# Kernel tuning notes

Measured on AMD Instinct MI355X. Metric: run time of the kernel, lower is better.

## Reference

```python
import jax, jax.numpy as jnp
import numpy as np
from jax import lax

B, H, W, C, K, R, CB = 2, 128, 128, 256, 64, 8, 256


def _conv(x, w, b=None, pad=1, lhs_dil=None, groups=1):
    out = lax.conv_general_dilated(x, w, (1, 1), [(pad, pad), (pad, pad)],
                                   lhs_dilation=lhs_dil, feature_group_count=groups,
                                   dimension_numbers=('NCHW', 'OIHW', 'NCHW'))
    return out if b is None else out + b[None, :, None, None]


def _silu(x):
    return x * jax.nn.sigmoid(x)


def _fuse(l0, l1, l2, p1w, p1b, p2w, p3w):
    # proj1: Conv(k=3)+SiLU (BN folded); proj2/proj3: grouped ConvTranspose2d as lhs-dilated grouped convs
    a = _silu(_conv(l0, p1w, p1b))
    b2 = _conv(l1, p2w, pad=2, lhs_dil=(2, 2), groups=CB)  # ConvT(2CB->CB, k4, s2, p1, g=CB)
    b3 = _conv(l2, p3w, pad=5, lhs_dil=(4, 4), groups=CB)  # ConvT(4CB->CB, k8, s4, p2, g=CB)
    return a + b2 + b3


def _corr_map(emb, trk):
    # emb: [H,W,C], trk: [K,C]; cosine-similarity correlation with local argmax radius masking
    e = emb / jnp.maximum(jnp.linalg.norm(emb, axis=-1, keepdims=True), 1e-12)
    t = trk / jnp.maximum(jnp.linalg.norm(trk, axis=-1, keepdims=True), 1e-12)
    y = jnp.maximum(jnp.einsum('hwc,kc->khw', e, t), 0.0)  # torch.where(y>0, y, 0)
    idx = jnp.argmax(y.reshape(K, -1), axis=1)             # first max, like torch.nonzero(...)[0]
    ai, aj = idx // W, idx % W
    rows = jnp.arange(H)[None, :, None]
    cols = jnp.arange(W)[None, None, :]
    m = ((rows >= (ai[:, None, None] - R)) & (rows < (ai[:, None, None] + R)) &
         (cols >= (aj[:, None, None] - R)) & (cols < (aj[:, None, None] + R)))
    s = jnp.sum(y * m, axis=0)
    return s / jnp.max(s)


def setup_inputs():
    key = jax.random.key(0)
    ks = jax.random.split(key, 32)
    r = lambda i, shp, s=0.02: jax.random.normal(ks[i], shp, jnp.float32) * s
    z = lambda n: jnp.zeros((n,), jnp.float32)
    return dict(
        id_embeding=jax.random.normal(ks[0], (B, H, W, C), jnp.float32),
        tracklets=jax.random.normal(ks[1], (B, K, C), jnp.float32),
        l0=jax.random.normal(ks[2], (B, CB, H, W), jnp.float32),
        l1=jax.random.normal(ks[3], (B, 2 * CB, H // 2, W // 2), jnp.float32),
        l2=jax.random.normal(ks[4], (B, 4 * CB, H // 4, W // 4), jnp.float32),
        b_p1w=r(5, (CB, CB, 3, 3)), b_p1b=z(CB),
        b_p2w=r(6, (CB, 2, 4, 4)), b_p3w=r(7, (CB, 4, 8, 8)),
        b_c1w=r(8, (CB, CB, 3, 3)), b_c1b=z(CB),
        b_c2w=r(9, (4, CB, 3, 3)), b_c2b=z(4),
        h_p1w=r(10, (CB, CB, 3, 3)), h_p1b=z(CB),
        h_p2w=r(11, (CB, 2, 4, 4)), h_p3w=r(12, (CB, 4, 8, 8)),
        h_c1aw=r(13, (CB, 1, 3, 3), 0.1), h_c1ab=z(CB),
        h_c1bw=r(14, (1, CB, 3, 3)), h_c1bb=z(1),
        h_c2aw=r(15, (CB, CB, 3, 3)), h_c2ab=z(CB),
        h_c2bw=r(16, (CB, CB, 3, 3)), h_c2bb=z(CB),
        h_c2cw=r(17, (1, CB, 3, 3)), h_c2cb=z(1),
    )


def reference(id_embeding, tracklets, l0, l1, l2,
              b_p1w, b_p1b, b_p2w, b_p3w, b_c1w, b_c1b, b_c2w, b_c2b,
              h_p1w, h_p1b, h_p2w, h_p3w,
              h_c1aw, h_c1ab, h_c1bw, h_c1bb,
              h_c2aw, h_c2ab, h_c2bw, h_c2bb, h_c2cw, h_c2cb):
    # correlation map per batch -> x_F [B,1,H,W]
    x_F = jax.vmap(_corr_map)(id_embeding, tracklets)[:, None]
    # recheck_Box head
    xd_box = _fuse(l0, l1, l2, b_p1w, b_p1b, b_p2w, b_p3w)
    xb = _silu(_conv(xd_box, b_c1w, b_c1b))
    siambox = jnp.transpose(_conv(xb, b_c2w, b_c2b), (0, 2, 3, 1))  # [B,H,W,4]
    # recheck_heatmap head
    xd_hm = _fuse(l0, l1, l2, h_p1w, h_p1b, h_p2w, h_p3w)
    xf = _conv(_silu(_conv(x_F, h_c1aw, h_c1ab)), h_c1bw, h_c1bb)   # [B,1,H,W]
    t = xf * xd_hm                                                  # broadcast over CB channels
    t = _silu(_conv(t, h_c2aw, h_c2ab))
    t = _silu(_conv(t, h_c2bw, h_c2bb))
    hmmap = jax.nn.sigmoid(_conv(t, h_c2cw, h_c2cb))                # [B,1,H,W]
    return (hmmap, siambox)
```

## Files before the change

kernel.cpp:

```cpp
#include <hip/hip_runtime.h>
#include <math.h>

#define HH 128
#define WW 128
#define HWSZ 16384
#define CC 256
#define KK 64
#define BB 2

typedef __bf16 bf16x8_t __attribute__((ext_vector_type(8)));
typedef float  f32x4_t  __attribute__((ext_vector_type(4)));

__device__ __forceinline__ float silu_f(float v) { return v / (1.f + expf(-v)); }
__device__ __forceinline__ float sigm_f(float v) { return 1.f / (1.f + expf(-v)); }

__device__ __forceinline__ float b2f(unsigned short u) {
    union { unsigned int i; float f; } x; x.i = ((unsigned int)u) << 16; return x.f;
}
__device__ __forceinline__ unsigned short f2b(float f) {
    union { float f; unsigned int i; } x; x.f = f;
    unsigned int r = x.i + 0x7FFFu + ((x.i >> 16) & 1u);
    return (unsigned short)(r >> 16);
}
__device__ __forceinline__ float u2f(unsigned int u) {
    union { unsigned int i; float f; } x; x.i = u; return x.f;
}

__global__ __launch_bounds__(256) void cvt_nhwc_kernel(const float* __restrict__ in,
                                                       unsigned short* __restrict__ out) {
    __shared__ float T[32][128];
    const int tid = threadIdx.x;
    const int y = blockIdx.x & 127;
    const int b = blockIdx.x >> 7;
    const float* inb = in + (size_t)b * CC * HWSZ + y * 128;
    unsigned short* outb = out + ((size_t)b * HWSZ + (size_t)y * 128) * CC;

    for (int c0 = 0; c0 < CC; c0 += 32) {
        __syncthreads();
        {
            int cl = tid >> 3;
            int xq = tid & 7;
            const float4* src = (const float4*)(inb + (size_t)(c0 + cl) * HWSZ);
            float4* dst = (float4*)&T[cl][0];
            #pragma unroll
            for (int j = 0; j < 4; j++) dst[xq * 4 + j] = src[xq * 4 + j];
        }
        __syncthreads();
        {
            int x = tid & 127, ch = tid >> 7;
            union { unsigned short u[16]; uint4 v[2]; } pk;
            #pragma unroll
            for (int j = 0; j < 16; j++) pk.u[j] = f2b(T[ch * 16 + j][x]);
            uint4* dst = (uint4*)&outb[(size_t)x * CC + c0 + ch * 16];
            dst[0] = pk.v[0];
            dst[1] = pk.v[1];
        }
    }
}

#define WTSZ (9 * 8 * 256 * 32)
__global__ __launch_bounds__(256) void wprep5_kernel(const float* __restrict__ w0,
                                                     const float* __restrict__ w1,
                                                     const float* __restrict__ w2,
                                                     const float* __restrict__ w3,
                                                     const float* __restrict__ w4,
                                                     unsigned short* __restrict__ wtbase) {
    const float* ws[5] = {w0, w1, w2, w3, w4};
    int set = blockIdx.y;
    const float* w = ws[set];
    int idx = blockIdx.x * 256 + threadIdx.x;
    int e   = idx & 7;
    int co  = (idx >> 3) & 255;
    int g   = (idx >> 11) & 3;
    int v   = idx >> 13;
    int cb  = v / 9;
    int t   = v - cb * 9;
    wtbase[(size_t)set * WTSZ + idx] = f2b(w[((size_t)co * 256 + cb * 32 + g * 8 + e) * 9 + t]);
}

#define EPAD 260
__global__ __launch_bounds__(256) void ycorr_kernel(const float* __restrict__ emb,
                                                    const float* __restrict__ trk,
                                                    float* __restrict__ y) {
    __shared__ __align__(16) float E[64 * EPAD];
    __shared__ __align__(16) float T[64 * EPAD];
    __shared__ float SE[64];
    __shared__ float ST[64];

    const int tid = threadIdx.x;
    const int b   = blockIdx.y;
    const int hw0 = blockIdx.x * 64;

    const float4* esrc = (const float4*)(emb + ((size_t)b * HWSZ + hw0) * CC);
    #pragma unroll
    for (int i = 0; i < 16; i++) {
        int q  = tid + i * 256;
        int px = q >> 6, c4 = q & 63;
        *(float4*)&E[px * EPAD + c4 * 4] = esrc[(size_t)px * 64 + c4];
    }
    const float4* tsrc = (const float4*)(trk + (size_t)b * KK * CC);
    #pragma unroll
    for (int i = 0; i < 16; i++) {
        int q = tid + i * 256;
        int k = q >> 6, c4 = q & 63;
        *(float4*)&T[k * EPAD + c4 * 4] = tsrc[(size_t)k * 64 + c4];
    }
    __syncthreads();

    if (tid < 64) {
        float ss = 0.f;
        const float4* ep = (const float4*)&E[tid * EPAD];
        #pragma unroll 8
        for (int c4 = 0; c4 < 64; c4++) {
            float4 v = ep[c4];
            ss += v.x * v.x + v.y * v.y + v.z * v.z + v.w * v.w;
        }
        SE[tid] = 1.f / fmaxf(sqrtf(ss), 1e-12f);
    } else if (tid < 128) {
        float ss = 0.f;
        const float4* tp = (const float4*)&T[(tid - 64) * EPAD];
        #pragma unroll 8
        for (int c4 = 0; c4 < 64; c4++) {
            float4 v = tp[c4];
            ss += v.x * v.x + v.y * v.y + v.z * v.z + v.w * v.w;
        }
        ST[tid - 64] = 1.f / fmaxf(sqrtf(ss), 1e-12f);
    }
    __syncthreads();

    const int pg = tid & 15;
    const int kg = tid >> 4;

    float acc[4][4];
    #pragma unroll
    for (int jp = 0; jp < 4; jp++)
        #pragma unroll
        for (int jk = 0; jk < 4; jk++) acc[jp][jk] = 0.f;

    const float* Ep[4];
    const float* Tp[4];
    #pragma unroll
    for (int jp = 0; jp < 4; jp++) Ep[jp] = &E[(jp * 16 + pg) * EPAD];
    #pragma unroll
    for (int jk = 0; jk < 4; jk++) Tp[jk] = &T[(jk * 16 + kg) * EPAD];

    #pragma unroll 2
    for (int c4 = 0; c4 < 64; ++c4) {
        float4 e[4], t[4];
        #pragma unroll
        for (int jp = 0; jp < 4; jp++) e[jp] = *(const float4*)(Ep[jp] + c4 * 4);
        #pragma unroll
        for (int jk = 0; jk < 4; jk++) t[jk] = *(const float4*)(Tp[jk] + c4 * 4);
        #define DOT4(a, t) (fmaf(a.w, t.w, fmaf(a.z, t.z, fmaf(a.y, t.y, a.x * t.x))))
        #pragma unroll
        for (int jp = 0; jp < 4; jp++)
            #pragma unroll
            for (int jk = 0; jk < 4; jk++)
                acc[jp][jk] += DOT4(e[jp], t[jk]);
        #undef DOT4
    }

    #pragma unroll
    for (int jp = 0; jp < 4; jp++) {
        int px = jp * 16 + pg;
        float se = SE[px];
        #pragma unroll
        for (int jk = 0; jk < 4; jk++) {
            int k = jk * 16 + kg;
            y[((size_t)b * KK + k) * HWSZ + hw0 + px] = fmaxf(acc[jp][jk], 0.f) * se * ST[k];
        }
    }
}

__global__ __launch_bounds__(256) void argmax_kernel(const float* __restrict__ y,
                                                     int* __restrict__ idxout,
                                                     unsigned int* __restrict__ umax) {
    int bk = blockIdx.x;
    int t = threadIdx.x;
    if (bk == 0 && t < BB) umax[t] = 0u;
    const float* p = y + (size_t)bk * HWSZ;
    float best = -1.f; int bi = 1 << 30;
    for (int i = t; i < HWSZ; i += 256) {
        float v = p[i];
        if (v > best) { best = v; bi = i; }
    }
    __shared__ float sv[256];
    __shared__ int   si[256];
    sv[t] = best; si[t] = bi;
    __syncthreads();
    for (int s = 128; s > 0; s >>= 1) {
        if (t < s) {
            float v2 = sv[t + s]; int i2 = si[t + s];
            if (v2 > sv[t] || (v2 == sv[t] && i2 < si[t])) { sv[t] = v2; si[t] = i2; }
        }
        __syncthreads();
    }
    if (t == 0) idxout[bk] = si[0];
}

__global__ __launch_bounds__(256) void smap_kernel(const float* __restrict__ y,
                                                   const int* __restrict__ idx,
                                                   float* __restrict__ s,
                                                   unsigned int* __restrict__ umax) {
    int b  = blockIdx.y;
    int hw = blockIdx.x * 256 + threadIdx.x;
    int h  = hw >> 7, w = hw & 127;
    __shared__ int ai[KK], aj[KK];
    if (threadIdx.x < KK) {
        int v = idx[b * KK + threadIdx.x];
        ai[threadIdx.x] = v >> 7;
        aj[threadIdx.x] = v & 127;
    }
    __syncthreads();
    const float* yb = y + (size_t)b * KK * HWSZ;
    float acc = 0.f;
    #pragma unroll 8
    for (int k = 0; k < KK; k++) {
        float v = yb[(size_t)k * HWSZ + hw];
        bool in = (h >= ai[k] - 8) && (h < ai[k] + 8) && (w >= aj[k] - 8) && (w < aj[k] + 8);
        acc += in ? v : 0.f;
    }
    s[(size_t)b * HWSZ + hw] = acc;

    __shared__ float sm[256];
    sm[threadIdx.x] = acc;
    __syncthreads();
    for (int st = 128; st > 0; st >>= 1) {
        if (threadIdx.x < st) sm[threadIdx.x] = fmaxf(sm[threadIdx.x], sm[threadIdx.x + st]);
        __syncthreads();
    }
    if (threadIdx.x == 0) {
        union { float f; unsigned int i; } x; x.f = sm[0];
        atomicMax(&umax[b], x.i);
    }
}

template <int HEADS>
__global__ __launch_bounds__(256) void deconv_kernel(const float* __restrict__ l1,
                                                     const float* __restrict__ l2,
                                                     const float* __restrict__ w2a,
                                                     const float* __restrict__ w3a,
                                                     const float* __restrict__ w2b,
                                                     const float* __restrict__ w3b,
                                                     unsigned short* __restrict__ outA,
                                                     unsigned short* __restrict__ outB) {
    __shared__ float L1[2][64][64];
    __shared__ float L2[4][32][32];

    const int tid = threadIdx.x;
    const int g   = blockIdx.x & 255;
    const int b   = blockIdx.x >> 8;

    const float4* l1b = (const float4*)(l1 + ((size_t)b * 2 * CC + 2 * g) * 4096);
    float4* L1p = (float4*)&L1[0][0][0];
    #pragma unroll
    for (int i = 0; i < 8; i++) L1p[tid + i * 256] = l1b[tid + i * 256];
    const float4* l2b = (const float4*)(l2 + ((size_t)b * 4 * CC + 4 * g) * 1024);
    float4* L2p = (float4*)&L2[0][0][0];
    #pragma unroll
    for (int i = 0; i < 4; i++) L2p[tid + i * 256] = l2b[tid + i * 256];

    const int x    = tid & 127;
    const int ytop = tid >> 7;

    const int pxo = x & 1, pyo = ytop & 1;
    const int mx0 = (x + pxo - 2) >> 1;
    const int dy2 = (ytop + pyo - 2) >> 1;
    const bool nok0 = (unsigned)mx0 < 64u;
    const bool nok1 = (unsigned)(mx0 + 1) < 64u;
    const int nc0 = mx0 & 63, nc1 = (mx0 + 1) & 63;

    const int px3 = (5 - (x & 3)) & 3;
    const int n30 = (x + px3 - 5) >> 2;
    const bool n3ok0 = (unsigned)n30 < 32u;
    const bool n3ok1 = (unsigned)(n30 + 1) < 32u;
    const int n3c0 = n30 & 31, n3c1 = (n30 + 1) & 31;
    int dy3[2], py3v[2];
    #pragma unroll
    for (int ph = 0; ph < 2; ph++) {
        int py3 = (5 - ((ytop + 2 * ph) & 3)) & 3;
        py3v[ph] = py3;
        dy3[ph] = (2 * ph + ytop + py3 - 5) >> 2;
    }

    __syncthreads();

    const float* w2s[2] = {w2a, w2b};
    const float* w3s[2] = {w3a, w3b};
    unsigned short* outs[2] = {outA, outB};

    #pragma unroll 1
    for (int hd = 0; hd < HEADS; ++hd) {
        const float* w2g = w2s[hd] + (size_t)g * 32;
        const float* w3g = w3s[hd] + (size_t)g * 256;

        float W2[2][2][2];
        #pragma unroll
        for (int ci = 0; ci < 2; ci++)
            #pragma unroll
            for (int a = 0; a < 2; a++)
                #pragma unroll
                for (int c = 0; c < 2; c++)
                    W2[ci][a][c] = w2g[ci * 16 + (pyo + 2 * a) * 4 + (pxo + 2 * c)];
        float W3[2][4][2][2];
        #pragma unroll
        for (int ph = 0; ph < 2; ph++)
            #pragma unroll
            for (int ci = 0; ci < 4; ci++)
                #pragma unroll
                for (int a = 0; a < 2; a++)
                    #pragma unroll
                    for (int c = 0; c < 2; c++)
                        W3[ph][ci][a][c] = w3g[ci * 64 + (py3v[ph] + 4 * a) * 8 + (px3 + 4 * c)];

        unsigned short* outb = outs[hd] + ((size_t)b * CC + g) * HWSZ;

        #pragma unroll 2
        for (int ii = 0; ii < 32; ++ii) {
            #pragma unroll
            for (int ph = 0; ph < 2; ph++) {
                const int i = 2 * ii + ph;
                float acc = 0.f;
                {
                    const int m0 = i + dy2;
                    #pragma unroll
                    for (int a = 0; a < 2; a++) {
                        int m = m0 + a;
                        bool mok = (unsigned)m < 64u;
                        int mc = m & 63;
                        #pragma unroll
                        for (int ci = 0; ci < 2; ci++) {
                            float v0 = (mok && nok0) ? L1[ci][mc][nc0] : 0.f;
                            float v1 = (mok && nok1) ? L1[ci][mc][nc1] : 0.f;
                            acc = fmaf(W2[ci][a][0], v0, acc);
                            acc = fmaf(W2[ci][a][1], v1, acc);
                        }
                    }
                }
                {
                    const int m0 = ii + dy3[ph];
                    #pragma unroll
                    for (int a = 0; a < 2; a++) {
                        int m = m0 + a;
                        bool mok = (unsigned)m < 32u;
                        int mc = m & 31;
                        #pragma unroll
                        for (int ci = 0; ci < 4; ci++) {
                            float v0 = (mok && n3ok0) ? L2[ci][mc][n3c0] : 0.f;
                            float v1 = (mok && n3ok1) ? L2[ci][mc][n3c1] : 0.f;
                            acc = fmaf(W3[ph][ci][a][0], v0, acc);
                            acc = fmaf(W3[ph][ci][a][1], v1, acc);
                        }
                    }
                }
                outb[(size_t)i * 256 + tid] = f2b(acc);
            }
        }
    }
}

template <int ADDB, int MULF>
__device__ __forceinline__ void conv_mfma_body(
    int y0, int co0, int b,
    const unsigned short* __restrict__ in,
    const unsigned short* __restrict__ wt,
    const float* __restrict__ bias,
    const unsigned short* __restrict__ addb,
    const float* __restrict__ xf,
    unsigned short* __restrict__ out,
    unsigned short (*Alds)[3 * 130 * 32])
{
    const int tid  = threadIdx.x;
    const int lane = tid & 63;
    const int wv   = tid >> 6;
    const int wco  = wv >> 1;
    const int wpx  = wv & 1;
    const int l15  = lane & 15;
    const int kg   = lane >> 4;

    const unsigned short* inb = in + (size_t)b * HWSZ * CC;
    const float* xfb = MULF ? (xf + (size_t)b * HWSZ) : nullptr;
    const unsigned short* wp = wt + (size_t)kg * 2048 + (size_t)(co0 + wco * 64 + l15) * 8;

    int ach[3][4];
    #pragma unroll
    for (int tl = 0; tl < 3; tl++)
        #pragma unroll
        for (int f = 0; f < 4; f++) {
            int px = wpx * 64 + f * 16 + l15 + tl;
            ach[tl][f] = (px * 4 + (kg ^ ((px >> 1) & 3))) * 8;
        }

    f32x4_t acc[4][4];
    #pragma unroll
    for (int i = 0; i < 4; i++)
        #pragma unroll
        for (int j = 0; j < 4; j++)
            acc[i][j] = (f32x4_t){0.f, 0.f, 0.f, 0.f};

    if (tid < 48) {
        int q4 = tid & 3;
        int hp = (tid >> 2) & 1;
        int r  = (tid >> 3) % 3;
        int bi = tid / 24;
        int px = hp ? 129 : 0;
        int chunk = (r * 130 + px) * 4 + (q4 ^ ((px >> 1) & 3));
        *reinterpret_cast<uint4*>(&Alds[bi][chunk * 8]) = make_uint4(0u, 0u, 0u, 0u);
    }

    uint4 streg[6];
    float sxf[6];

    auto load_A = [&](int cb) {
        #pragma unroll
        for (int i = 0; i < 6; i++) {
            int q   = tid + i * 256;
            int q4  = q & 3;
            int pxi = (q >> 2) & 127;
            int r   = q >> 9;
            int gy  = y0 - 1 + r;
            uint4 v = make_uint4(0u, 0u, 0u, 0u);
            float fxv = 0.f;
            if ((unsigned)gy < 128u) {
                v = *reinterpret_cast<const uint4*>(
                        inb + ((size_t)(gy * 128 + pxi)) * CC + cb * 32 + q4 * 8);
                if (MULF) fxv = xfb[gy * 128 + pxi];
            }
            streg[i] = v;
            if (MULF) sxf[i] = fxv;
        }
    };
    auto write_A = [&](int bufi) {
        #pragma unroll
        for (int i = 0; i < 6; i++) {
            int q   = tid + i * 256;
            int q4  = q & 3;
            int pxi = (q >> 2) & 127;
            int r   = q >> 9;
            int px  = pxi + 1;
            int chunk = (r * 130 + px) * 4 + (q4 ^ ((px >> 1) & 3));
            uint4 v = streg[i];
            if (MULF) {
                union { unsigned short u[8]; uint4 w; } pk;
                pk.w = v;
                float fm = sxf[i];
                #pragma unroll
                for (int e = 0; e < 8; e++) pk.u[e] = f2b(b2f(pk.u[e]) * fm);
                v = pk.w;
            }
            *reinterpret_cast<uint4*>(&Alds[bufi][chunk * 8]) = v;
        }
    };

    load_A(0);
    write_A(0);

    bf16x8_t W[3][4], P[2][4];
    #pragma unroll
    for (int f = 0; f < 4; f++) W[0][f] = *reinterpret_cast<const bf16x8_t*>(wp + f * 128);
    #pragma unroll
    for (int f = 0; f < 4; f++) W[1][f] = *reinterpret_cast<const bf16x8_t*>(wp + 8192 + f * 128);

    __syncthreads();
    #pragma unroll
    for (int f = 0; f < 4; f++)
        P[0][f] = *reinterpret_cast<const bf16x8_t*>(&Alds[0][ach[0][f]]);

    for (int cb = 0; cb < 8; ++cb) {
        const int bufi = cb & 1;
        if (cb + 1 < 8) load_A(cb + 1);
        const unsigned short* wcb = wp + (size_t)cb * 73728;
        #pragma unroll
        for (int t = 0; t < 9; ++t) {
            if (cb < 7 || t < 7) {
                #pragma unroll
                for (int f = 0; f < 4; f++)
                    W[(t + 2) % 3][f] = *reinterpret_cast<const bf16x8_t*>(
                        wcb + (t + 2) * 8192 + f * 128);
            }
            if (t < 8) {
                const int aoff = ((t + 1) / 3) * 4160;
                #pragma unroll
                for (int f = 0; f < 4; f++)
                    P[(t + 1) & 1][f] = *reinterpret_cast<const bf16x8_t*>(
                        &Alds[bufi][aoff + ach[(t + 1) % 3][f]]);
            }
            __builtin_amdgcn_sched_barrier(0);
            #pragma unroll
            for (int cf = 0; cf < 4; cf++)
                #pragma unroll
                for (int pf = 0; pf < 4; pf++)
                    acc[cf][pf] = __builtin_amdgcn_mfma_f32_16x16x32_bf16(
                        W[t % 3][cf], P[t & 1][pf], acc[cf][pf], 0, 0, 0);
        }
        if (cb + 1 < 8) write_A(bufi ^ 1);
        __syncthreads();
        if (cb + 1 < 8) {
            #pragma unroll
            for (int f = 0; f < 4; f++)
                P[0][f] = *reinterpret_cast<const bf16x8_t*>(&Alds[(cb + 1) & 1][ach[0][f]]);
        }
    }

    size_t outB = ((size_t)b * HWSZ + (size_t)y0 * 128) * CC;
    #pragma unroll
    for (int cf = 0; cf < 4; cf++) {
        int co = co0 + wco * 64 + cf * 16 + kg * 4;
        float bs0 = bias[co], bs1 = bias[co + 1], bs2 = bias[co + 2], bs3 = bias[co + 3];
        #pragma unroll
        for (int pf = 0; pf < 4; pf++) {
            int x = wpx * 64 + pf * 16 + l15;
            float v0 = silu_f(acc[cf][pf][0] + bs0);
            float v1 = silu_f(acc[cf][pf][1] + bs1);
            float v2 = silu_f(acc[cf][pf][2] + bs2);
            float v3 = silu_f(acc[cf][pf][3] + bs3);
            if (ADDB) {
                size_t ab = ((size_t)b * CC + co) * HWSZ + (size_t)y0 * 128 + x;
                v0 += b2f(addb[ab]);
                v1 += b2f(addb[ab + HWSZ]);
                v2 += b2f(addb[ab + 2 * HWSZ]);
                v3 += b2f(addb[ab + 3 * HWSZ]);
            }
            union { unsigned short u[4]; uint2 v; } pk;
            pk.u[0] = f2b(v0); pk.u[1] = f2b(v1); pk.u[2] = f2b(v2); pk.u[3] = f2b(v3);
            *reinterpret_cast<uint2*>(&out[outB + (size_t)x * CC + co]) = pk.v;
        }
    }
}

template <int ADDB, int MULF>
__global__ __launch_bounds__(256, 2) void conv_mfma_kernel(
    const unsigned short* __restrict__ in,
    const unsigned short* __restrict__ wt,
    const float* __restrict__ bias,
    const unsigned short* __restrict__ addb,
    const float* __restrict__ xf,
    unsigned short* __restrict__ out)
{
    __shared__ __align__(16) unsigned short Alds[2][3 * 130 * 32];
    const int l   = (blockIdx.x & 7) * 64 + (blockIdx.x >> 3);
    const int y0  = l >> 2;
    const int co0 = ((l >> 1) & 1) * 128;
    const int b   = l & 1;
    conv_mfma_body<ADDB, MULF>(y0, co0, b, in, wt, bias, addb, xf, out, Alds);
}

__global__ __launch_bounds__(256, 2) void conv_mfma_dual_kernel(
    const unsigned short* __restrict__ in,
    const unsigned short* __restrict__ wt2set,
    const float* __restrict__ biasB,
    const float* __restrict__ biasH,
    const unsigned short* __restrict__ addbB,
    const unsigned short* __restrict__ addbH,
    unsigned short* __restrict__ outB,
    unsigned short* __restrict__ outH)
{
    __shared__ __align__(16) unsigned short Alds[2][3 * 130 * 32];
    const int l    = (blockIdx.x & 7) * 128 + (blockIdx.x >> 3);
    const int y0   = l >> 3;
    const int c3   = l & 7;
    const int head = c3 >> 2;
    const int co0  = ((c3 >> 1) & 1) * 128;
    const int b    = c3 & 1;
    conv_mfma_body<1, 0>(y0, co0, b,
                         in,
                         wt2set + (size_t)head * WTSZ,
                         head ? biasH : biasB,
                         head ? addbH : addbB,
                         nullptr,
                         head ? outH : outB,
                         Alds);
}

__global__ __launch_bounds__(256) void conv_c1a_kernel(const float* __restrict__ s,
                                                       const unsigned int* __restrict__ umax,
                                                       const float* __restrict__ w,
                                                       const float* __restrict__ bias,
                                                       unsigned short* __restrict__ out) {
    __shared__ float W[2304];
    __shared__ float S[3][34];

    const int tid = threadIdx.x;
    const int idx = blockIdx.x;
    const int b   = idx >> 9;
    const int seg = idx & 511;
    const int y   = seg >> 2;
    const int x0  = (seg & 3) * 32;

    for (int i = tid; i < 2304; i += 256) W[i] = w[i];
    if (tid < 102) {
        int r = tid / 34, xx = tid - r * 34;
        int gy = y - 1 + r, gx = x0 - 1 + xx;
        S[r][xx] = ((unsigned)gy < 128u && (unsigned)gx < 128u)
                       ? s[(size_t)b * HWSZ + gy * 128 + gx] : 0.f;
    }
    __syncthreads();

    const float im = 1.f / u2f(umax[b]);
    const int cog = tid >> 5;
    const int px  = tid & 31;

    float sv[9];
    #pragma unroll
    for (int r = 0; r < 3; r++)
        #pragma unroll
        for (int d = 0; d < 3; d++)
            sv[r * 3 + d] = S[r][px + d];

    unsigned short* op =
        &out[((size_t)b * HWSZ + (size_t)y * 128 + x0 + px) * CC + cog * 32];
    #pragma unroll
    for (int q = 0; q < 4; q++) {
        union { unsigned short u[8]; uint4 v; } pk;
        #pragma unroll
        for (int j = 0; j < 8; j++) {
            int co = cog * 32 + q * 8 + j;
            float a = 0.f;
            #pragma unroll
            for (int t = 0; t < 9; t++) a = fmaf(W[co * 9 + t], sv[t], a);
            pk.u[j] = f2b(silu_f(a * im + bias[co]));
        }
        *reinterpret_cast<uint4*>(op + q * 8) = pk.v;
    }
}

template <int COUT, int MODE>
__global__ __launch_bounds__(256) void small_conv_kernel(
    const unsigned short* __restrict__ in,
    const float* __restrict__ w,
    const float* __restrict__ bias,
    float* __restrict__ out)
{
    __shared__ float WL[COUT * 9 * 32 * 12];

    const int tid = threadIdx.x;
    for (int i = tid; i < COUT * 2304; i += 256) {
        int e = i & 7;
        int g = (i >> 3) & 31;
        int rest = i >> 8;
        int t = rest % 9;
        int co = rest / 9;
        WL[((co * 9 + t) * 32 + g) * 12 + e] = w[((size_t)co * 256 + g * 8 + e) * 9 + t];
    }
    __syncthreads();

    const int lane = tid & 63;
    const int wv   = tid >> 6;
    const int c32  = lane & 31;
    const int ps   = lane >> 5;
    const int grp  = blockIdx.x * 4 + wv;
    const int base = grp * 4;
    const int b    = base >> 14;
    const int pix  = base & (HWSZ - 1);
    const int y    = pix >> 7;
    const int x0   = pix & 127;
    const int p0x  = x0 + 2 * ps;

    const unsigned short* inb = in + (size_t)b * HWSZ * CC;

    uint4 d[3][4];
    #pragma unroll
    for (int r = 0; r < 3; r++) {
        int gy = y - 1 + r;
        #pragma unroll
        for (int cx = 0; cx < 4; cx++) {
            int gx = p0x - 1 + cx;
            uint4 v = make_uint4(0u, 0u, 0u, 0u);
            if ((unsigned)gy < 128u && (unsigned)gx < 128u)
                v = *reinterpret_cast<const uint4*>(
                        inb + ((size_t)(gy * 128 + gx)) * CC + c32 * 8);
            d[r][cx] = v;
        }
    }

    float acc[2][COUT];
    #pragma unroll
    for (int p = 0; p < 2; p++)
        #pragma unroll
        for (int c = 0; c < COUT; c++) acc[p][c] = 0.f;

    #pragma unroll
    for (int r = 0; r < 3; r++) {
        float f[4][8];
        #pragma unroll
        for (int cx = 0; cx < 4; cx++) {
            union { unsigned short u[8]; uint4 v; } pk;
            pk.v = d[r][cx];
            #pragma unroll
            for (int e = 0; e < 8; e++) f[cx][e] = b2f(pk.u[e]);
        }
        #pragma unroll
        for (int dx = 0; dx < 3; dx++) {
            #pragma unroll
            for (int co = 0; co < COUT; co++) {
                int bse = ((co * 9 + r * 3 + dx) * 32 + c32) * 12;
                float4 wa = *(const float4*)&WL[bse];
                float4 wb = *(const float4*)&WL[bse + 4];
                #pragma unroll
                for (int p = 0; p < 2; p++) {
                    const float* ff = f[dx + p];
                    float a = acc[p][co];
                    a = fmaf(ff[0], wa.x, a); a = fmaf(ff[1], wa.y, a);
                    a = fmaf(ff[2], wa.z, a); a = fmaf(ff[3], wa.w, a);
                    a = fmaf(ff[4], wb.x, a); a = fmaf(ff[5], wb.y, a);
                    a = fmaf(ff[6], wb.z, a); a = fmaf(ff[7], wb.w, a);
                    acc[p][co] = a;
                }
            }
        }
    }

    #pragma unroll
    for (int m = 1; m <= 16; m <<= 1)
        #pragma unroll
        for (int p = 0; p < 2; p++)
            #pragma unroll
            for (int co = 0; co < COUT; co++)
                acc[p][co] += __shfl_xor(acc[p][co], m);

    if (c32 == 0) {
        #pragma unroll
        for (int p = 0; p < 2; p++) {
            size_t pixidx = (size_t)base + 2 * ps + p;
            if (MODE == 0) {
                ((float4*)out)[pixidx] = make_float4(
                    acc[p][0] + bias[0],
                    acc[p][COUT > 1 ? 1 : 0] + bias[COUT > 1 ? 1 : 0],
                    acc[p][COUT > 2 ? 2 : 0] + bias[COUT > 2 ? 2 : 0],
                    acc[p][COUT > 3 ? 3 : 0] + bias[COUT > 3 ? 3 : 0]);
            } else if (MODE == 1) {
                out[pixidx] = acc[p][0] + bias[0];
            } else {
                out[pixidx] = sigm_f(acc[p][0] + bias[0]);
            }
        }
    }
}

extern "C" void kernel_launch(void* const* d_in, const int* in_sizes, int n_in,
                              void* d_out, int out_size, void* d_ws, size_t ws_size,
                              hipStream_t stream) {
    const float* emb    = (const float*)d_in[0];
    const float* trk    = (const float*)d_in[1];
    const float* l0     = (const float*)d_in[2];
    const float* l1     = (const float*)d_in[3];
    const float* l2     = (const float*)d_in[4];
    const float* b_p1w  = (const float*)d_in[5];
    const float* b_p1b  = (const float*)d_in[6];
    const float* b_p2w  = (const float*)d_in[7];
    const float* b_p3w  = (const float*)d_in[8];
    const float* b_c1w  = (const float*)d_in[9];
    const float* b_c1b  = (const float*)d_in[10];
    const float* b_c2w  = (const float*)d_in[11];
    const float* b_c2b  = (const float*)d_in[12];
    const float* h_p1w  = (const float*)d_in[13];
    const float* h_p1b  = (const float*)d_in[14];
    const float* h_p2w  = (const float*)d_in[15];
    const float* h_p3w  = (const float*)d_in[16];
    const float* h_c1aw = (const float*)d_in[17];
    const float* h_c1ab = (const float*)d_in[18];
    const float* h_c1bw = (const float*)d_in[19];
    const float* h_c1bb = (const float*)d_in[20];
    const float* h_c2aw = (const float*)d_in[21];
    const float* h_c2ab = (const float*)d_in[22];
    const float* h_c2bw = (const float*)d_in[23];
    const float* h_c2bb = (const float*)d_in[24];
    const float* h_c2cw = (const float*)d_in[25];
    const float* h_c2cb = (const float*)d_in[26];

    float* outp = (float*)d_out;

    const size_t ACT = (size_t)BB * CC * HWSZ;
    const size_t WT  = (size_t)WTSZ;
    const size_t SMALLS = 131400;

    unsigned short* l0nh = (unsigned short*)d_ws;
    unsigned short* wtP  = l0nh + ACT;
    unsigned short* bufA = wtP + 5 * WT;
    unsigned short* bufB = bufA + ACT;
    unsigned short* bufC = bufB + ACT;
    float* sbuf   = (float*)(bufC + ACT);
    float* xfb    = sbuf + (size_t)BB * HWSZ;
    unsigned int* umax = (unsigned int*)(xfb + (size_t)BB * HWSZ);
    int*   idxb   = (int*)(umax + 2);
    unsigned short* bufD = bufC + ACT + SMALLS;
    float* ybuf   = (float*)bufB;

    const size_t NEED = (size_t)(bufD + ACT - l0nh) * sizeof(unsigned short);
    const bool fast = ws_size >= NEED;

    cvt_nhwc_kernel<<<BB * 128, 256, 0, stream>>>(l0, l0nh);
    wprep5_kernel<<<dim3((unsigned)(WT / 256), 5), 256, 0, stream>>>(
        b_p1w, h_p1w, b_c1w, h_c2aw, h_c2bw, wtP);

    ycorr_kernel<<<dim3(256, BB), 256, 0, stream>>>(emb, trk, ybuf);
    argmax_kernel<<<BB * KK, 256, 0, stream>>>(ybuf, idxb, umax);
    smap_kernel<<<dim3(64, BB), 256, 0, stream>>>(ybuf, idxb, sbuf, umax);

    if (fast) {
        deconv_kernel<2><<<BB * CC, 256, 0, stream>>>(l1, l2, b_p2w, b_p3w, h_p2w, h_p3w,
                                                      bufA, bufD);
        conv_mfma_dual_kernel<<<1024, 256, 0, stream>>>(l0nh, wtP, b_p1b, h_p1b,
                                                        bufA, bufD, bufB, bufC);
        conv_mfma_kernel<0, 0><<<512, 256, 0, stream>>>(bufB, wtP + 2 * WT, b_c1b,
                                                        nullptr, nullptr, bufA);
        small_conv_kernel<4, 0><<<2048, 256, 0, stream>>>(bufA, b_c2w, b_c2b,
                                                          outp + BB * HWSZ);
        conv_c1a_kernel<<<1024, 256, 0, stream>>>(sbuf, umax, h_c1aw, h_c1ab, bufB);
        small_conv_kernel<1, 1><<<2048, 256, 0, stream>>>(bufB, h_c1bw, h_c1bb, xfb);
        conv_mfma_kernel<0, 1><<<512, 256, 0, stream>>>(bufC, wtP + 3 * WT, h_c2ab,
                                                        nullptr, xfb, bufA);
        conv_mfma_kernel<0, 0><<<512, 256, 0, stream>>>(bufA, wtP + 4 * WT, h_c2bb,
                                                        nullptr, nullptr, bufB);
        small_conv_kernel<1, 2><<<2048, 256, 0, stream>>>(bufB, h_c2cw, h_c2cb, outp);
    } else {
        deconv_kernel<1><<<BB * CC, 256, 0, stream>>>(l1, l2, b_p2w, b_p3w,
                                                      nullptr, nullptr, bufA, nullptr);
        conv_mfma_kernel<1, 0><<<512, 256, 0, stream>>>(l0nh, wtP, b_p1b, bufA,
                                                        nullptr, bufB);
        conv_mfma_kernel<0, 0><<<512, 256, 0, stream>>>(bufB, wtP + 2 * WT, b_c1b,
                                                        nullptr, nullptr, bufC);
        small_conv_kernel<4, 0><<<2048, 256, 0, stream>>>(bufC, b_c2w, b_c2b,
                                                          outp + BB * HWSZ);
        deconv_kernel<1><<<BB * CC, 256, 0, stream>>>(l1, l2, h_p2w, h_p3w,
                                                      nullptr, nullptr, bufA, nullptr);
        conv_mfma_kernel<1, 0><<<512, 256, 0, stream>>>(l0nh, wtP + 1 * WT, h_p1b, bufA,
                                                        nullptr, bufB);
        conv_c1a_kernel<<<1024, 256, 0, stream>>>(sbuf, umax, h_c1aw, h_c1ab, bufC);
        small_conv_kernel<1, 1><<<2048, 256, 0, stream>>>(bufC, h_c1bw, h_c1bb, xfb);
        conv_mfma_kernel<0, 1><<<512, 256, 0, stream>>>(bufB, wtP + 3 * WT, h_c2ab,
                                                        nullptr, xfb, bufA);
        conv_mfma_kernel<0, 0><<<512, 256, 0, stream>>>(bufA, wtP + 4 * WT, h_c2bb,
                                                        nullptr, nullptr, bufC);
        small_conv_kernel<1, 2><<<2048, 256, 0, stream>>>(bufC, h_c2cw, h_c2cb, outp);
    }
}
```

Before: 400.3 us.

## Merge two independent 3x3 MFMA convs into one launch and single-buffer LDS

Adds a combined kernel that runs the box-head c1 conv and the heatmap-head c2a conv (with the xf multiply) in one 1024-block grid, reordering the launch sequence so the xf producers run first. The A-tile LDS staging buffer drops from double to single buffering, with extra barriers around the write, which halves shared memory per block to raise occupancy. The cost is that global-to-LDS writes no longer overlap MFMA work from the previous channel block, so there are more synchronisation stalls.

```diff
diff --git a/kernel.cpp b/kernel.cpp
--- a/kernel.cpp
+++ b/kernel.cpp
@@ -368,7 +368,7 @@
     const unsigned short* __restrict__ addb,
     const float* __restrict__ xf,
     unsigned short* __restrict__ out,
-    unsigned short (*Alds)[3 * 130 * 32])
+    unsigned short* __restrict__ Alds)
 {
     const int tid  = threadIdx.x;
     const int lane = tid & 63;
@@ -398,14 +398,13 @@
         for (int j = 0; j < 4; j++)
             acc[i][j] = (f32x4_t){0.f, 0.f, 0.f, 0.f};
 
-    if (tid < 48) {
+    if (tid < 24) {
         int q4 = tid & 3;
         int hp = (tid >> 2) & 1;
-        int r  = (tid >> 3) % 3;
-        int bi = tid / 24;
+        int r  = tid >> 3;
         int px = hp ? 129 : 0;
         int chunk = (r * 130 + px) * 4 + (q4 ^ ((px >> 1) & 3));
-        *reinterpret_cast<uint4*>(&Alds[bi][chunk * 8]) = make_uint4(0u, 0u, 0u, 0u);
+        *reinterpret_cast<uint4*>(&Alds[chunk * 8]) = make_uint4(0u, 0u, 0u, 0u);
     }
 
     uint4 streg[6];
@@ -430,7 +429,7 @@
             if (MULF) sxf[i] = fxv;
         }
     };
-    auto write_A = [&](int bufi) {
+    auto write_A = [&]() {
         #pragma unroll
         for (int i = 0; i < 6; i++) {
             int q   = tid + i * 256;
@@ -448,12 +447,12 @@
                 for (int e = 0; e < 8; e++) pk.u[e] = f2b(b2f(pk.u[e]) * fm);
                 v = pk.w;
             }
-            *reinterpret_cast<uint4*>(&Alds[bufi][chunk * 8]) = v;
+            *reinterpret_cast<uint4*>(&Alds[chunk * 8]) = v;
         }
     };
 
     load_A(0);
-    write_A(0);
+    write_A();
 
     bf16x8_t W[3][4], P[2][4];
     #pragma unroll
@@ -464,10 +463,9 @@
     __syncthreads();
     #pragma unroll
     for (int f = 0; f < 4; f++)
-        P[0][f] = *reinterpret_cast<const bf16x8_t*>(&Alds[0][ach[0][f]]);
+        P[0][f] = *reinterpret_cast<const bf16x8_t*>(&Alds[ach[0][f]]);
 
     for (int cb = 0; cb < 8; ++cb) {
-        const int bufi = cb & 1;
         if (cb + 1 < 8) load_A(cb + 1);
         const unsigned short* wcb = wp + (size_t)cb * 73728;
         #pragma unroll
@@ -483,7 +481,7 @@
                 #pragma unroll
                 for (int f = 0; f < 4; f++)
                     P[(t + 1) & 1][f] = *reinterpret_cast<const bf16x8_t*>(
-                        &Alds[bufi][aoff + ach[(t + 1) % 3][f]]);
+                        &Alds[aoff + ach[(t + 1) % 3][f]]);
             }
             __builtin_amdgcn_sched_barrier(0);
             #pragma unroll
@@ -493,12 +491,13 @@
                     acc[cf][pf] = __builtin_amdgcn_mfma_f32_16x16x32_bf16(
                         W[t % 3][cf], P[t & 1][pf], acc[cf][pf], 0, 0, 0);
         }
-        if (cb + 1 < 8) write_A(bufi ^ 1);
-        __syncthreads();
         if (cb + 1 < 8) {
+            __syncthreads();
+            write_A();
+            __syncthreads();
             #pragma unroll
             for (int f = 0; f < 4; f++)
-                P[0][f] = *reinterpret_cast<const bf16x8_t*>(&Alds[(cb + 1) & 1][ach[0][f]]);
+                P[0][f] = *reinterpret_cast<const bf16x8_t*>(&Alds[ach[0][f]]);
         }
     }
 
@@ -537,7 +536,7 @@
     const float* __restrict__ xf,
     unsigned short* __restrict__ out)
 {
-    __shared__ __align__(16) unsigned short Alds[2][3 * 130 * 32];
+    __shared__ __align__(16) unsigned short Alds[3 * 130 * 32];
     const int l   = (blockIdx.x & 7) * 64 + (blockIdx.x >> 3);
     const int y0  = l >> 2;
     const int co0 = ((l >> 1) & 1) * 128;
@@ -555,7 +554,7 @@
     unsigned short* __restrict__ outB,
     unsigned short* __restrict__ outH)
 {
-    __shared__ __align__(16) unsigned short Alds[2][3 * 130 * 32];
+    __shared__ __align__(16) unsigned short Alds[3 * 130 * 32];
     const int l    = (blockIdx.x & 7) * 128 + (blockIdx.x >> 3);
     const int y0   = l >> 3;
     const int c3   = l & 7;
@@ -570,6 +569,30 @@
                          nullptr,
                          head ? outH : outB,
                          Alds);
+}
+
+__global__ __launch_bounds__(256, 2) void conv_mfma_dualmix_kernel(
+    const unsigned short* __restrict__ in0,
+    const unsigned short* __restrict__ in1,
+    const unsigned short* __restrict__ wt0,
+    const unsigned short* __restrict__ wt1,
+    const float* __restrict__ bias0,
+    const float* __restrict__ bias1,
+    const float* __restrict__ xf,
+    unsigned short* __restrict__ out0,
+    unsigned short* __restrict__ out1)
+{
+    __shared__ __align__(16) unsigned short Alds[3 * 130 * 32];
+    const int l    = (blockIdx.x & 7) * 128 + (blockIdx.x >> 3);
+    const int y0   = l >> 3;
+    const int c3   = l & 7;
+    const int head = c3 >> 2;
+    const int co0  = ((c3 >> 1) & 1) * 128;
+    const int b    = c3 & 1;
+    if (head == 0)
+        conv_mfma_body<0, 0>(y0, co0, b, in0, wt0, bias0, nullptr, nullptr, out0, Alds);
+    else
+        conv_mfma_body<0, 1>(y0, co0, b, in1, wt1, bias1, nullptr, xf, out1, Alds);
 }
 
 __global__ __launch_bounds__(256) void conv_c1a_kernel(const float* __restrict__ s,
@@ -802,14 +825,14 @@
                                                       bufA, bufD);
         conv_mfma_dual_kernel<<<1024, 256, 0, stream>>>(l0nh, wtP, b_p1b, h_p1b,
                                                         bufA, bufD, bufB, bufC);
-        conv_mfma_kernel<0, 0><<<512, 256, 0, stream>>>(bufB, wtP + 2 * WT, b_c1b,
-                                                        nullptr, nullptr, bufA);
-        small_conv_kernel<4, 0><<<2048, 256, 0, stream>>>(bufA, b_c2w, b_c2b,
+        conv_c1a_kernel<<<1024, 256, 0, stream>>>(sbuf, umax, h_c1aw, h_c1ab, bufA);
+        small_conv_kernel<1, 1><<<2048, 256, 0, stream>>>(bufA, h_c1bw, h_c1bb, xfb);
+        conv_mfma_dualmix_kernel<<<1024, 256, 0, stream>>>(bufB, bufC,
+                                                           wtP + 2 * WT, wtP + 3 * WT,
+                                                           b_c1b, h_c2ab, xfb,
+                                                           bufD, bufA);
+        small_conv_kernel<4, 0><<<2048, 256, 0, stream>>>(bufD, b_c2w, b_c2b,
                                                           outp + BB * HWSZ);
-        conv_c1a_kernel<<<1024, 256, 0, stream>>>(sbuf, umax, h_c1aw, h_c1ab, bufB);
-        small_conv_kernel<1, 1><<<2048, 256, 0, stream>>>(bufB, h_c1bw, h_c1bb, xfb);
-        conv_mfma_kernel<0, 1><<<512, 256, 0, stream>>>(bufC, wtP + 3 * WT, h_c2ab,
-                                                        nullptr, xfb, bufA);
         conv_mfma_kernel<0, 0><<<512, 256, 0, stream>>>(bufA, wtP + 4 * WT, h_c2bb,
                                                         nullptr, nullptr, bufB);
         small_conv_kernel<1, 2><<<2048, 256, 0, stream>>>(bufB, h_c2cw, h_c2cb, outp);
```

Measured after the change: 407.7 us. Within noise of the previous version (+1.9%).
